# Performance work log

Hardware: AMD Instinct MI355X
Metric: run time of the kernel (lower is better)

The kernel has to match this reference:

```python
import jax, jax.numpy as jnp
import numpy as np

B, T, C, H = 4, 4096, 1024, 128

def setup_inputs() -> dict:
    key = jax.random.key(0)
    k1, k2, k3, k4 = jax.random.split(key, 4)
    s = 1.0 / np.sqrt(C)  # roughly match nn.Linear init scale
    return {
        "xd": jax.random.normal(k1, (B, T, C), dtype=jnp.float32),
        "Wq": jax.random.normal(k2, (C, H), dtype=jnp.float32) * s,
        "Wk": jax.random.normal(k3, (C, H), dtype=jnp.float32) * s,
        "Wv": jax.random.normal(k4, (C, H), dtype=jnp.float32) * s,
    }

def reference(xd, Wq, Wk, Wv):
    # self-attention path (xe is None): k, q, v all from xd
    q = jnp.einsum("btc,ch->bth", xd, Wq)
    k = jnp.einsum("btc,ch->bth", xd, Wk)
    v = jnp.einsum("btc,ch->bth", xd, Wv)
    scale = jnp.asarray(k.shape[-1], q.dtype) ** -0.5
    wei = jnp.einsum("bqh,bkh->bqk", q, k) * scale  # [B, T, T]
    # causal mask (masking=True): tril == 0 -> -inf
    causal = jnp.tril(jnp.ones((xd.shape[1], xd.shape[1]), dtype=bool))
    wei = jnp.where(causal[None, :, :], wei, jnp.asarray(-jnp.inf, wei.dtype))
    wei = jax.nn.softmax(wei, axis=-1)
    # dropout: eval-mode identity (deterministic reference)
    out = jnp.einsum("bqk,bkh->bqh", wei, v)  # [B, T, H]
    return out
```

## Files before the change

### kernel.cpp

```cpp
#include <hip/hip_runtime.h>
#include <math.h>

typedef __bf16 bf16x8 __attribute__((ext_vector_type(8)));
typedef float f32x4 __attribute__((ext_vector_type(4)));
typedef float f32x16 __attribute__((ext_vector_type(16)));
typedef unsigned int u32x4 __attribute__((ext_vector_type(4)));
typedef unsigned short u16x8 __attribute__((ext_vector_type(8)));

#define B_ 4
#define T_ 4096
#define C_ 1024
#define H_ 128

static __device__ __forceinline__ unsigned short f32_to_bf16(float f) {
  unsigned int u = __builtin_bit_cast(unsigned int, f);
  u += 0x7FFFu + ((u >> 16) & 1u);
  return (unsigned short)(u >> 16);
}
static __device__ __forceinline__ float bf16_to_f32(unsigned short u) {
  unsigned int x = ((unsigned int)u) << 16;
  return __builtin_bit_cast(float, x);
}

static __device__ __forceinline__ bf16x8 ld16g(const unsigned short* p) {
  return __builtin_bit_cast(bf16x8, *(const u32x4*)p);
}

static __device__ __forceinline__ f32x4 mfma16(bf16x8 a, bf16x8 b, f32x4 c) {
  return __builtin_amdgcn_mfma_f32_16x16x32_bf16(a, b, c, 0, 0, 0);
}
static __device__ __forceinline__ f32x16 mfma32(bf16x8 a, bf16x8 b, f32x16 c) {
  return __builtin_amdgcn_mfma_f32_32x32x16_bf16(a, b, c, 0, 0, 0);
}

static __device__ __forceinline__ void swapu(unsigned int& a, unsigned int& b) {
  asm volatile("v_permlane32_swap_b32 %0, %1" : "+v"(a), "+v"(b));
}
static __device__ __forceinline__ unsigned int cvtpk(float lo, float hi) {
  unsigned int r;
  asm("v_cvt_pk_bf16_f32 %0, %1, %2" : "=v"(r) : "v"(lo), "v"(hi));
  return r;
}
static __device__ __forceinline__ unsigned short cvt1(float v) {
  return (unsigned short)cvtpk(v, v);
}
static __device__ __forceinline__ float bpermf(int addr, float v) {
  return __builtin_bit_cast(float, __builtin_amdgcn_ds_bpermute(addr, __builtin_bit_cast(int, v)));
}
static __device__ __forceinline__ float half_merge_max(float x) {
  return fmaxf(x, __shfl_xor(x, 32));
}
static __device__ __forceinline__ float half_merge_sum(float x) {
  return x + __shfl_xor(x, 32);
}
static __device__ __forceinline__ float vmax16(f32x16 v) {
  float a0 = fmaxf(v[0], v[1]),  a1 = fmaxf(v[2], v[3]);
  float a2 = fmaxf(v[4], v[5]),  a3 = fmaxf(v[6], v[7]);
  float a4 = fmaxf(v[8], v[9]),  a5 = fmaxf(v[10], v[11]);
  float a6 = fmaxf(v[12], v[13]), a7 = fmaxf(v[14], v[15]);
  float b0 = fmaxf(a0, a1), b1 = fmaxf(a2, a3), b2 = fmaxf(a4, a5), b3 = fmaxf(a6, a7);
  return fmaxf(fmaxf(b0, b1), fmaxf(b2, b3));
}
static __device__ __forceinline__ float vsum16(f32x16 v) {
  float a0 = v[0] + v[1],  a1 = v[2] + v[3],  a2 = v[4] + v[5],  a3 = v[6] + v[7];
  float a4 = v[8] + v[9],  a5 = v[10] + v[11], a6 = v[12] + v[13], a7 = v[14] + v[15];
  float b0 = a0 + a1, b1 = a2 + a3, b2 = a4 + a5, b3 = a6 + a7;
  return (b0 + b1) + (b2 + b3);
}

typedef __attribute__((address_space(1))) const unsigned char as1_u8;
typedef __attribute__((address_space(3))) unsigned char as3_u8;
static __device__ __forceinline__ void async16(const void* g, void* l) {
  __builtin_amdgcn_global_load_lds((as1_u8*)g, (as3_u8*)l, 16, 0, 0);
}

static __device__ __forceinline__ u16x8 pack8cvt(float4 a, float4 b) {
  u32x4 u;
  u[0] = cvtpk(a.x, a.y); u[1] = cvtpk(a.z, a.w);
  u[2] = cvtpk(b.x, b.y); u[3] = cvtpk(b.z, b.w);
  return __builtin_bit_cast(u16x8, u);
}

#define PART_BYTES 33792

__global__ __launch_bounds__(256) void conv_w_kernel(const float* __restrict__ W0,
                                                     const float* __restrict__ W1,
                                                     const float* __restrict__ W2,
                                                     unsigned short* __restrict__ WT,
                                                     float qscale) {
  int tid = blockIdx.x * 256 + threadIdx.x;
  int o = tid >> 17;
  int r = tid & 131071;
  int n = r & 127;
  int k = r >> 7;
  const float* W = (o == 0) ? W0 : ((o == 1) ? W1 : W2);
  float v = W[r];
  if (o == 0) v *= qscale;
  WT[(size_t)o * 131072 + (size_t)n * 1024 + k] = f32_to_bf16(v);
}

__global__ __launch_bounds__(256) void qkv_fused_kernel(const float* __restrict__ X,
                                                        const unsigned short* __restrict__ WT,
                                                        unsigned short* __restrict__ Qb,
                                                        unsigned short* __restrict__ K3,
                                                        unsigned short* __restrict__ V3) {
  __shared__ __align__(16) unsigned short At[128 * 64];
  __shared__ __align__(16) unsigned short Bt[192 * 64];
  const int bid = blockIdx.x;
  const int xcd = bid & 7, u = bid >> 3;
  const int ch = u & 1;
  const int rt = (u >> 1) * 8 + xcd;

  const float* Ax = X + (size_t)rt * 128 * 1024;
  const unsigned short* Bsrc = WT + (size_t)ch * 192 * 1024;

  const int tid = threadIdx.x;
  const int lane = tid & 63, wid = tid >> 6;
  const int l15 = lane & 15, lg = lane >> 4;
  const int srow = wid * 8 + (lane >> 3);
  const int scol = (lane & 7) * 8;
  const int swcol = scol ^ ((srow & 7) << 3);
  const int sbcol = (((lane & 7) ^ (lane >> 3)) << 3);
  const int wm = wid >> 1, wn = wid & 1;
  const int rsw = (l15 & 7) << 3;

  const f32x4 fzero = {0.f, 0.f, 0.f, 0.f};
  f32x4 acc[4][6];
#pragma unroll
  for (int i = 0; i < 4; i++)
#pragma unroll
    for (int j = 0; j < 6; j++) acc[i][j] = fzero;

  float4 fA[4][2];
#pragma unroll
  for (int i4 = 0; i4 < 4; i4++) {
    const float* xs = Ax + (size_t)(i4 * 32 + srow) * 1024 + scol;
    fA[i4][0] = *(const float4*)xs;
    fA[i4][1] = *(const float4*)(xs + 4);
  }

  for (int ks = 0; ks < 16; ks++) {
    const int k0 = ks * 64;
    __syncthreads();
#pragma unroll
    for (int i6 = 0; i6 < 6; i6++)
      async16(Bsrc + (size_t)(i6 * 32 + srow) * 1024 + k0 + sbcol, &Bt[(i6 * 32 + wid * 8) * 64]);
#pragma unroll
    for (int i4 = 0; i4 < 4; i4++) {
      const int row = i4 * 32 + srow;
      *(u16x8*)(&At[row * 64 + swcol]) = pack8cvt(fA[i4][0], fA[i4][1]);
    }
    __syncthreads();
    if (ks + 1 < 16) {
#pragma unroll
      for (int i4 = 0; i4 < 4; i4++) {
        const float* xs = Ax + (size_t)(i4 * 32 + srow) * 1024 + (ks + 1) * 64 + scol;
        fA[i4][0] = *(const float4*)xs;
        fA[i4][1] = *(const float4*)(xs + 4);
      }
    }
#pragma unroll
    for (int kk = 0; kk < 2; kk++) {
      bf16x8 af[4], bfr[6];
#pragma unroll
      for (int i = 0; i < 4; i++)
        af[i] = ld16g(&At[(wm * 64 + i * 16 + l15) * 64 + ((kk * 32 + lg * 8) ^ rsw)]);
#pragma unroll
      for (int j = 0; j < 6; j++)
        bfr[j] = ld16g(&Bt[(wn * 96 + j * 16 + l15) * 64 + ((kk * 32 + lg * 8) ^ rsw)]);
      __builtin_amdgcn_s_setprio(1);
#pragma unroll
      for (int i = 0; i < 4; i++)
#pragma unroll
        for (int j = 0; j < 6; j++) acc[i][j] = mfma16(af[i], bfr[j], acc[i][j]);
      __builtin_amdgcn_s_setprio(0);
    }
  }

#pragma unroll
  for (int j = 0; j < 6; j++) {
    const int nb = ch * 192 + wn * 96 + j * 16;
    const int o = nb >> 7;
    const int dbase = nb & 127;
    if (o == 0) {
#pragma unroll
      for (int i = 0; i < 4; i++)
#pragma unroll
        for (int r = 0; r < 4; r++) {
          int row = rt * 128 + wm * 64 + i * 16 + lg * 4 + r;
          int col = dbase + l15;
          Qb[(size_t)row * 128 + col] = cvt1(acc[i][j][r]);
        }
    } else if (o == 1) {
#pragma unroll
      for (int i = 0; i < 4; i++)
#pragma unroll
        for (int r = 0; r < 4; r++) {
          int token = rt * 128 + wm * 64 + i * 16 + lg * 4 + r;
          int d = dbase + l15;
          int bb = token >> 12, t = token & 4095;
          int t32 = t >> 5;
          int lane2 = (t & 31) | (((d >> 3) & 1) << 5);
          int c = d >> 4;
          int j2 = d & 7;
          K3[(size_t)(((bb * 128 + t32) * 8 + c) * 64 + lane2) * 8 + j2] = cvt1(acc[i][j][r]);
        }
    } else {
#pragma unroll
      for (int i = 0; i < 4; i++)
#pragma unroll
        for (int r = 0; r < 4; r++) {
          int token = rt * 128 + wm * 64 + i * 16 + lg * 4 + r;
          int d = dbase + l15;
          int bb = token >> 12, tt = token & 4095;
          int t32 = tt >> 5;
          int kss = (tt >> 4) & 1;
          int hi2 = (tt >> 3) & 1;
          int j2 = tt & 7;
          int dt = d >> 5;
          int lane2 = (d & 31) | (hi2 << 5);
          V3[(size_t)(((bb * 128 + t32) * 8 + dt * 2 + kss) * 64 + lane2) * 8 + j2] = cvt1(acc[i][j][r]);
        }
    }
  }
}

__global__ __launch_bounds__(256, 2) void attn_kernel(const unsigned short* __restrict__ Qb,
                                                      const unsigned short* __restrict__ K3,
                                                      const unsigned short* __restrict__ V3,
                                                      unsigned char* __restrict__ Pw8) {
  const int bid = blockIdx.x;
  const int xcd = bid & 7;
  const int b = xcd >> 1;
  const int rest = bid >> 3;
  const int h = rest % 6;
  const int jj = rest / 6;
  const int g = (xcd & 1) + 2 * (15 - jj);

  const int tid = threadIdx.x;
  const int wid = tid >> 6, lane = tid & 63;
  const int l31 = lane & 31, hi = lane >> 5;
  const int qbase = g * 128 + wid * 32;

  __shared__ __align__(16) unsigned char LDSraw[32768];
  unsigned short* lbuf = (unsigned short*)LDSraw;

  const unsigned short* K3b = K3 + (size_t)b * 524288;
  const unsigned short* V3b = V3 + (size_t)b * 524288;
  const int jmax_w = 4 * g + wid;
  const int Jcap = 4 * g + 3;
  const int R = (Jcap >= h) ? ((Jcap - h) / 6 + 1) : 0;

  const unsigned short* qp = Qb + ((size_t)(b * T_ + qbase + l31) << 7) + hi * 8;
  bf16x8 qf[8];
#pragma unroll
  for (int c = 0; c < 8; c++) qf[c] = ld16g(qp + c * 16);

  const f32x16 z16 = {0.f,0.f,0.f,0.f,0.f,0.f,0.f,0.f,0.f,0.f,0.f,0.f,0.f,0.f,0.f,0.f};
  f32x16 o[4];
  o[0] = z16; o[1] = z16; o[2] = z16; o[3] = z16;
  float m = -1e30f, l = 0.f;
  const int addrbase = hi << 4;

  const unsigned short* sbase = (wid < 2) ? K3b : V3b;
  const int soff = (wid & 1) * 2048;
  const int region = ((wid >= 2) ? 4096 : 0) + soff;

  if (R > 0) {
    const unsigned short* s0 = sbase + (size_t)h * 4096 + soff + lane * 8;
    unsigned short* d0 = lbuf + region;
#pragma unroll
    for (int i = 0; i < 4; i++) async16(s0 + i * 512, d0 + i * 512);
  }

  for (int r = 0; r < R; r++) {
    const int cur = r & 1;
    if (r + 1 < R) {
      const int jS = h + 6 * (r + 1);
      const unsigned short* sN = sbase + (size_t)jS * 4096 + soff + lane * 8;
      unsigned short* dN = lbuf + (cur ^ 1) * 8192 + region;
#pragma unroll
      for (int i = 0; i < 4; i++) async16(sN + i * 512, dN + i * 512);
      asm volatile("s_waitcnt vmcnt(4)" ::: "memory");
    } else {
      asm volatile("s_waitcnt vmcnt(0)" ::: "memory");
    }
    __builtin_amdgcn_s_barrier();

    const int j = h + 6 * r;
    if (j <= jmax_w) {
      const unsigned short* Kl = lbuf + cur * 8192;
      const unsigned short* Vl = Kl + 4096;
      bf16x8 kf[8];
#pragma unroll
      for (int c = 0; c < 8; c++) kf[c] = ld16g(Kl + c * 512 + lane * 8);
      f32x16 s = z16;
      __builtin_amdgcn_s_setprio(1);
#pragma unroll
      for (int c = 0; c < 8; c++) s = mfma32(kf[c], qf[c], s);
      __builtin_amdgcn_s_setprio(0);

      bf16x8 vf[4][2];
#pragma unroll
      for (int dt = 0; dt < 4; dt++)
#pragma unroll
        for (int ks = 0; ks < 2; ks++)
          vf[dt][ks] = ld16g(Vl + (dt * 2 + ks) * 512 + lane * 8);

      if (j == jmax_w) {
        const int kvb = j << 5;
        const int qq = qbase + l31;
#pragma unroll
        for (int r2 = 0; r2 < 16; r2++) {
          const int c0 = (r2 & 3) + 8 * (r2 >> 2) + 4 * hi;
          if (kvb + c0 > qq) s[r2] = -1e30f;
        }
      }

      float pm = half_merge_max(vmax16(s));
      const bool skip = __all(pm - m <= 8.0f);
      float mn = skip ? m : fmaxf(m, pm);
#pragma unroll
      for (int r2 = 0; r2 < 16; r2++) s[r2] = exp2f(s[r2] - mn);
      float ps = half_merge_sum(vsum16(s));
      if (skip) {
        l = l + ps;
      } else {
        float al = exp2f(m - mn);
        m = mn;
        l = l * al + ps;
#pragma unroll
        for (int r2 = 0; r2 < 16; r2++) {
          const int addr = addrbase + 4 * ((r2 & 3) + 8 * (r2 >> 2));
          float alb = bpermf(addr, al);
          o[0][r2] *= alb; o[1][r2] *= alb; o[2][r2] *= alb; o[3][r2] *= alb;
        }
      }

      bf16x8 pa[2];
#pragma unroll
      for (int ks = 0; ks < 2; ks++) {
        const int gb = ks * 8;
        unsigned int xa = cvtpk(s[gb + 0], s[gb + 1]), xb = cvtpk(s[gb + 4], s[gb + 5]);
        swapu(xa, xb);
        unsigned int ya = cvtpk(s[gb + 2], s[gb + 3]), yb = cvtpk(s[gb + 6], s[gb + 7]);
        swapu(ya, yb);
        u32x4 pw; pw[0] = xa; pw[1] = ya; pw[2] = xb; pw[3] = yb;
        pa[ks] = __builtin_bit_cast(bf16x8, pw);
      }

      __builtin_amdgcn_s_setprio(1);
#pragma unroll
      for (int ks = 0; ks < 2; ks++)
#pragma unroll
        for (int dt = 0; dt < 4; dt++) o[dt] = mfma32(pa[ks], vf[dt][ks], o[dt]);
      __builtin_amdgcn_s_setprio(0);
    }
    __builtin_amdgcn_sched_barrier(0);
    __builtin_amdgcn_s_barrier();
  }

  unsigned char* Pb = Pw8 + (size_t)((b * 32 + g) * 6 + h) * PART_BYTES;
  unsigned short* Po = (unsigned short*)Pb;
  float* Pm = (float*)(Pb + 32768);
  float* Pl = (float*)(Pb + 33280);
#pragma unroll
  for (int r2 = 0; r2 < 16; r2++) {
    const int q128 = wid * 32 + (r2 & 3) + 8 * (r2 >> 2) + 4 * hi;
#pragma unroll
    for (int dt = 0; dt < 4; dt++)
      Po[q128 * 128 + dt * 32 + l31] = cvt1(o[dt][r2]);
  }
  if (lane < 32) { Pm[wid * 32 + l31] = m; Pl[wid * 32 + l31] = l; }
}

__global__ __launch_bounds__(256) void attn_merge_kernel(const unsigned char* __restrict__ Pw8,
                                                         float* __restrict__ Out) {
  const int bid = blockIdx.x;
  const int xcd = bid & 7, idx = bid >> 3;
  const int b = xcd >> 1;
  const int g = ((idx >> 4) << 1) | (xcd & 1);
  const int tl = b * 32 + g;
  const int inner = (idx & 15) * 256 + threadIdx.x;
  const int q = inner >> 5;
  const int d = (inner & 31) * 4;
  const unsigned char* base = Pw8 + (size_t)tl * 6 * PART_BYTES;

  float mm[6], ll[6];
#pragma unroll
  for (int p = 0; p < 6; p++) {
    mm[p] = *(const float*)(base + p * PART_BYTES + 32768 + q * 4);
    ll[p] = *(const float*)(base + p * PART_BYTES + 33280 + q * 4);
  }
  float mn = mm[0];
#pragma unroll
  for (int p = 1; p < 6; p++) mn = fmaxf(mn, mm[p]);
  float f[6], denom = 0.f;
#pragma unroll
  for (int p = 0; p < 6; p++) { f[p] = exp2f(mm[p] - mn); denom += f[p] * ll[p]; }
  const float inv = 1.0f / denom;

  f32x4 acc = {0.f, 0.f, 0.f, 0.f};
#pragma unroll
  for (int p = 0; p < 6; p++) {
    const unsigned short* po = (const unsigned short*)(base + p * PART_BYTES) + q * 128 + d;
    unsigned long long v4 = *(const unsigned long long*)po;
    const unsigned short* pv = (const unsigned short*)&v4;
#pragma unroll
    for (int i = 0; i < 4; i++) acc[i] += f[p] * bf16_to_f32(pv[i]);
  }
#pragma unroll
  for (int i = 0; i < 4; i++) acc[i] *= inv;
  *(f32x4*)(Out + (size_t)(b * 4096 + g * 128 + q) * 128 + d) = acc;
}

extern "C" void kernel_launch(void* const* d_in, const int* in_sizes, int n_in,
                              void* d_out, int out_size, void* d_ws, size_t ws_size,
                              hipStream_t stream) {
  const float* X  = (const float*)d_in[0];
  const float* W0 = (const float*)d_in[1];
  const float* W1 = (const float*)d_in[2];
  const float* W2 = (const float*)d_in[3];
  float* Out = (float*)d_out;

  unsigned char* ws = (unsigned char*)d_ws;
  unsigned short* WT = (unsigned short*)(ws);
  unsigned char* Pw  = ws;
  unsigned short* Qb = (unsigned short*)(ws + 34078720);
  unsigned short* K3 = (unsigned short*)(ws + 38273024);
  unsigned short* V3 = (unsigned short*)(ws + 42467328);

  const float qscale = 1.4426950408889634f / sqrtf(128.0f);

  conv_w_kernel<<<dim3(1536), dim3(256), 0, stream>>>(W0, W1, W2, WT, qscale);
  qkv_fused_kernel<<<dim3(256), dim3(256), 0, stream>>>(X, WT, Qb, K3, V3);
  attn_kernel<<<dim3(768), dim3(256), 0, stream>>>(Qb, K3, V3, Pw);
  attn_merge_kernel<<<dim3(2048), dim3(256), 0, stream>>>(Pw, Out);
}
```

Measured before the change: 75.24 us.

## Retile QKV projection so each block computes all outputs for 64 rows

Changes the QKV GEMM so each block handles 64 tokens across all 384 Q/K/V columns with 512 threads, instead of 128 tokens across half the columns. This removes the duplicate read and bf16 conversion of the fp32 input activations that occurred when two blocks shared a row tile. In exchange, each block streams the entire weight matrix, uses larger shared memory, and has fewer MFMAs per A fragment.

```diff
diff --git a/kernel.cpp b/kernel.cpp
--- a/kernel.cpp
+++ b/kernel.cpp
@@ -99,78 +99,68 @@
   WT[(size_t)o * 131072 + (size_t)n * 1024 + k] = f32_to_bf16(v);
 }
 
-__global__ __launch_bounds__(256) void qkv_fused_kernel(const float* __restrict__ X,
+__global__ __launch_bounds__(512) void qkv_fused_kernel(const float* __restrict__ X,
                                                         const unsigned short* __restrict__ WT,
                                                         unsigned short* __restrict__ Qb,
                                                         unsigned short* __restrict__ K3,
                                                         unsigned short* __restrict__ V3) {
-  __shared__ __align__(16) unsigned short At[128 * 64];
-  __shared__ __align__(16) unsigned short Bt[192 * 64];
-  const int bid = blockIdx.x;
-  const int xcd = bid & 7, u = bid >> 3;
-  const int ch = u & 1;
-  const int rt = (u >> 1) * 8 + xcd;
-
-  const float* Ax = X + (size_t)rt * 128 * 1024;
-  const unsigned short* Bsrc = WT + (size_t)ch * 192 * 1024;
+  __shared__ __align__(16) unsigned short At[64 * 64];
+  __shared__ __align__(16) unsigned short Bt[384 * 64];
+  const int rt = blockIdx.x;
+
+  const float* Ax = X + (size_t)rt * 64 * 1024;
 
   const int tid = threadIdx.x;
   const int lane = tid & 63, wid = tid >> 6;
   const int l15 = lane & 15, lg = lane >> 4;
+  const int wm = wid >> 2, wn = wid & 3;
   const int srow = wid * 8 + (lane >> 3);
   const int scol = (lane & 7) * 8;
   const int swcol = scol ^ ((srow & 7) << 3);
   const int sbcol = (((lane & 7) ^ (lane >> 3)) << 3);
-  const int wm = wid >> 1, wn = wid & 1;
   const int rsw = (l15 & 7) << 3;
 
   const f32x4 fzero = {0.f, 0.f, 0.f, 0.f};
-  f32x4 acc[4][6];
-#pragma unroll
-  for (int i = 0; i < 4; i++)
+  f32x4 acc[2][6];
+#pragma unroll
+  for (int i = 0; i < 2; i++)
 #pragma unroll
     for (int j = 0; j < 6; j++) acc[i][j] = fzero;
 
-  float4 fA[4][2];
-#pragma unroll
-  for (int i4 = 0; i4 < 4; i4++) {
-    const float* xs = Ax + (size_t)(i4 * 32 + srow) * 1024 + scol;
-    fA[i4][0] = *(const float4*)xs;
-    fA[i4][1] = *(const float4*)(xs + 4);
+  float4 fA0, fA1;
+  {
+    const float* xs = Ax + (size_t)srow * 1024 + scol;
+    fA0 = *(const float4*)xs;
+    fA1 = *(const float4*)(xs + 4);
   }
 
   for (int ks = 0; ks < 16; ks++) {
     const int k0 = ks * 64;
     __syncthreads();
 #pragma unroll
-    for (int i6 = 0; i6 < 6; i6++)
-      async16(Bsrc + (size_t)(i6 * 32 + srow) * 1024 + k0 + sbcol, &Bt[(i6 * 32 + wid * 8) * 64]);
-#pragma unroll
-    for (int i4 = 0; i4 < 4; i4++) {
-      const int row = i4 * 32 + srow;
-      *(u16x8*)(&At[row * 64 + swcol]) = pack8cvt(fA[i4][0], fA[i4][1]);
-    }
+    for (int j = 0; j < 6; j++) {
+      const int row = wid * 48 + j * 8 + (lane >> 3);
+      async16(WT + (size_t)row * 1024 + k0 + sbcol, &Bt[(wid * 48 + j * 8) * 64]);
+    }
+    *(u16x8*)(&At[srow * 64 + swcol]) = pack8cvt(fA0, fA1);
     __syncthreads();
     if (ks + 1 < 16) {
-#pragma unroll
-      for (int i4 = 0; i4 < 4; i4++) {
-        const float* xs = Ax + (size_t)(i4 * 32 + srow) * 1024 + (ks + 1) * 64 + scol;
-        fA[i4][0] = *(const float4*)xs;
-        fA[i4][1] = *(const float4*)(xs + 4);
-      }
+      const float* xs = Ax + (size_t)srow * 1024 + (ks + 1) * 64 + scol;
+      fA0 = *(const float4*)xs;
+      fA1 = *(const float4*)(xs + 4);
     }
 #pragma unroll
     for (int kk = 0; kk < 2; kk++) {
-      bf16x8 af[4], bfr[6];
-#pragma unroll
-      for (int i = 0; i < 4; i++)
-        af[i] = ld16g(&At[(wm * 64 + i * 16 + l15) * 64 + ((kk * 32 + lg * 8) ^ rsw)]);
+      bf16x8 af[2], bfr[6];
+#pragma unroll
+      for (int i = 0; i < 2; i++)
+        af[i] = ld16g(&At[(wm * 32 + i * 16 + l15) * 64 + ((kk * 32 + lg * 8) ^ rsw)]);
 #pragma unroll
       for (int j = 0; j < 6; j++)
         bfr[j] = ld16g(&Bt[(wn * 96 + j * 16 + l15) * 64 + ((kk * 32 + lg * 8) ^ rsw)]);
       __builtin_amdgcn_s_setprio(1);
 #pragma unroll
-      for (int i = 0; i < 4; i++)
+      for (int i = 0; i < 2; i++)
 #pragma unroll
         for (int j = 0; j < 6; j++) acc[i][j] = mfma16(af[i], bfr[j], acc[i][j]);
       __builtin_amdgcn_s_setprio(0);
@@ -179,24 +169,24 @@
 
 #pragma unroll
   for (int j = 0; j < 6; j++) {
-    const int nb = ch * 192 + wn * 96 + j * 16;
+    const int nb = wn * 96 + j * 16;
     const int o = nb >> 7;
     const int dbase = nb & 127;
     if (o == 0) {
 #pragma unroll
-      for (int i = 0; i < 4; i++)
+      for (int i = 0; i < 2; i++)
 #pragma unroll
         for (int r = 0; r < 4; r++) {
-          int row = rt * 128 + wm * 64 + i * 16 + lg * 4 + r;
+          int row = rt * 64 + wm * 32 + i * 16 + lg * 4 + r;
           int col = dbase + l15;
           Qb[(size_t)row * 128 + col] = cvt1(acc[i][j][r]);
         }
     } else if (o == 1) {
 #pragma unroll
-      for (int i = 0; i < 4; i++)
+      for (int i = 0; i < 2; i++)
 #pragma unroll
         for (int r = 0; r < 4; r++) {
-          int token = rt * 128 + wm * 64 + i * 16 + lg * 4 + r;
+          int token = rt * 64 + wm * 32 + i * 16 + lg * 4 + r;
           int d = dbase + l15;
           int bb = token >> 12, t = token & 4095;
           int t32 = t >> 5;
@@ -207,10 +197,10 @@
         }
     } else {
 #pragma unroll
-      for (int i = 0; i < 4; i++)
+      for (int i = 0; i < 2; i++)
 #pragma unroll
         for (int r = 0; r < 4; r++) {
-          int token = rt * 128 + wm * 64 + i * 16 + lg * 4 + r;
+          int token = rt * 64 + wm * 32 + i * 16 + lg * 4 + r;
           int d = dbase + l15;
           int bb = token >> 12, tt = token & 4095;
           int t32 = tt >> 5;
@@ -433,7 +423,7 @@
   const float qscale = 1.4426950408889634f / sqrtf(128.0f);
 
   conv_w_kernel<<<dim3(1536), dim3(256), 0, stream>>>(W0, W1, W2, WT, qscale);
-  qkv_fused_kernel<<<dim3(256), dim3(256), 0, stream>>>(X, WT, Qb, K3, V3);
+  qkv_fused_kernel<<<dim3(256), dim3(512), 0, stream>>>(X, WT, Qb, K3, V3);
   attn_kernel<<<dim3(768), dim3(256), 0, stream>>>(Qb, K3, V3, Pw);
   attn_merge_kernel<<<dim3(2048), dim3(256), 0, stream>>>(Pw, Out);
 }
```

Result: no change. 74.66 us (-0.8%).
